# Kernel optimization log

Measured on AMD Instinct MI355X. Metric: run time of the kernel, lower is better.

The kernel has to match this reference:

```python
import jax, jax.numpy as jnp
import numpy as np

WT, WH, WW = 2, 8, 8
N_WIN = WT * WH * WW  # 128 tokens per window
DIM, HEADS = 192, 6
HEAD_DIM = DIM // HEADS
SCALE = HEAD_DIM ** -0.5


def _relative_position_index():
    ct, ch, cw = np.arange(WT), np.arange(WH), np.arange(WW)
    coords = np.stack(np.meshgrid(ct, ch, cw, indexing='ij'))  # (3,WT,WH,WW)
    cf = coords.reshape(3, -1)
    rel = cf[:, :, None] - cf[:, None, :]  # (3,N,N)
    rel = rel.transpose(1, 2, 0).copy()
    rel[:, :, 0] += WT - 1
    rel[:, :, 1] += WH - 1
    rel[:, :, 2] += WW - 1
    rel[:, :, 0] *= (2 * WH - 1) * (2 * WW - 1)
    rel[:, :, 1] *= 2 * WW - 1
    return rel.sum(-1)  # (N,N) int

_REL_IDX = jnp.asarray(_relative_position_index())


def _layernorm(x, g, b, eps=1e-5):
    mu = x.mean(-1, keepdims=True)
    var = ((x - mu) ** 2).mean(-1, keepdims=True)
    return (x - mu) * jax.lax.rsqrt(var + eps) * g + b


def setup_inputs() -> dict:
    key = jax.random.key(0)
    ks = jax.random.split(key, 16)
    B, T, H, W, C = 2, 8, 128, 128, DIM
    hid = 4 * C
    n_bias = (2 * WT - 1) * (2 * WH - 1) * (2 * WW - 1)
    s = lambda fan: 1.0 / np.sqrt(fan)
    return {
        'x': jax.random.normal(ks[0], (B, T, H, W, C), jnp.float32),
        'norm1_g': jnp.ones((C,), jnp.float32),
        'norm1_b': jnp.zeros((C,), jnp.float32),
        'qkv_w': jax.random.normal(ks[1], (3 * C, C), jnp.float32) * s(C),
        'qkv_b': jnp.zeros((3 * C,), jnp.float32),
        'bias_table': jax.random.normal(ks[2], (n_bias, HEADS), jnp.float32) * 0.02,
        'proj_w': jax.random.normal(ks[3], (C, C), jnp.float32) * s(C),
        'proj_b': jnp.zeros((C,), jnp.float32),
        'norm2_g': jnp.ones((C,), jnp.float32),
        'norm2_b': jnp.zeros((C,), jnp.float32),
        'fc1_w': jax.random.normal(ks[4], (hid, C), jnp.float32) * s(C),
        'fc1_b': jnp.zeros((hid,), jnp.float32),
        'fc2_w': jax.random.normal(ks[5], (C, hid), jnp.float32) * s(hid),
        'fc2_b': jnp.zeros((C,), jnp.float32),
    }


def reference(x, norm1_g, norm1_b, qkv_w, qkv_b, bias_table, proj_w, proj_b,
              norm2_g, norm2_b, fc1_w, fc1_b, fc2_w, fc2_b):
    B, T, H, W, C = x.shape
    shortcut = x
    xn = _layernorm(x, norm1_g, norm1_b)

    # window partition: (B,T,H,W,C) -> (B_, N, C)
    xw = xn.reshape(B, T // WT, WT, H // WH, WH, W // WW, WW, C)
    xw = xw.transpose(0, 1, 3, 5, 2, 4, 6, 7).reshape(-1, N_WIN, C)

    # qkv projection (torch Linear: y = x @ W.T + b)
    qkv = xw @ qkv_w.T + qkv_b  # (B_, N, 3C)
    B_ = qkv.shape[0]
    qkv = qkv.reshape(B_, N_WIN, 3, HEADS, HEAD_DIM)
    q, k, v = qkv[:, :, 0], qkv[:, :, 1], qkv[:, :, 2]  # (B_, N, h, d)

    attn = jnp.einsum('bnhd,bmhd->bhnm', q * SCALE, k)
    bias = bias_table[_REL_IDX.reshape(-1)].reshape(N_WIN, N_WIN, HEADS)
    attn = attn + bias.transpose(2, 0, 1)[None]  # (B_, h, N, N)
    attn = jax.nn.softmax(attn, axis=-1)

    out = jnp.einsum('bhnm,bmhd->bnhd', attn, v).reshape(B_, N_WIN, C)
    out = out @ proj_w.T + proj_b

    # window reverse
    out = out.reshape(B, T // WT, H // WH, W // WW, WT, WH, WW, C)
    out = out.transpose(0, 1, 4, 2, 5, 3, 6, 7).reshape(B, T, H, W, C)

    x = shortcut + out
    # MLP with residual (GELU exact, matching nn.GELU default)
    h1 = _layernorm(x, norm2_g, norm2_b) @ fc1_w.T + fc1_b
    h1 = jax.nn.gelu(h1, approximate=False)
    x = x + (h1 @ fc2_w.T + fc2_b)
    return x
```

## Files before the change

kernel.cpp:

```cpp
#include <hip/hip_runtime.h>
#include <hip/hip_bf16.h>
#include <math.h>

typedef __hip_bfloat16 bf16;
typedef __attribute__((ext_vector_type(8))) __bf16 bf16x8;
typedef __attribute__((ext_vector_type(4))) float floatx4;

#define CDIM 192
#define N_WINDOWS 2048
#define ATT_SCALE 0.17677669529663687f

__device__ inline float toF(float v) { return v; }
__device__ inline float toF(bf16 v) { return __bfloat162float(v); }

__device__ inline long nat_index(int wi, int n, int col) {
    int wb = wi & 15, hb = (wi >> 4) & 15, tb = (wi >> 8) & 3, bb = wi >> 10;
    int t  = tb * 2 + (n >> 6);
    int hh = hb * 8 + ((n >> 3) & 7);
    int w  = wb * 8 + (n & 7);
    return ((((long)(bb * 8 + t)) * 128 + hh) * 128 + w) * CDIM + col;
}

template<bool WINDOWED, typename T>
__launch_bounds__(256)
__global__ void ln_kernel(const T* __restrict__ x, const float* __restrict__ g,
                          const float* __restrict__ bta, bf16* __restrict__ out,
                          int wi_base) {
    int row = blockIdx.x * 4 + (threadIdx.x >> 6);
    int lane = threadIdx.x & 63;
    long src;
    if (WINDOWED) {
        src = nat_index(wi_base + (row >> 7), row & 127, 0);
    } else {
        src = (long)row * CDIM;
    }
    float v0 = toF(x[src + lane]);
    float v1 = toF(x[src + lane + 64]);
    float v2 = toF(x[src + lane + 128]);
    float s = v0 + v1 + v2;
    float sq = v0 * v0 + v1 * v1 + v2 * v2;
    #pragma unroll
    for (int o = 32; o > 0; o >>= 1) { s += __shfl_xor(s, o); sq += __shfl_xor(sq, o); }
    float mean = s * (1.0f / 192.0f);
    float var  = sq * (1.0f / 192.0f) - mean * mean;
    float rstd = rsqrtf(fmaxf(var, 0.0f) + 1e-5f);
    long dst = (long)row * CDIM;
    out[dst + lane]       = __float2bfloat16((v0 - mean) * rstd * g[lane]       + bta[lane]);
    out[dst + lane + 64]  = __float2bfloat16((v1 - mean) * rstd * g[lane + 64]  + bta[lane + 64]);
    out[dst + lane + 128] = __float2bfloat16((v2 - mean) * rstd * g[lane + 128] + bta[lane + 128]);
}

template<typename Epi>
__launch_bounds__(256)
__global__ void gemm_bt(const bf16* __restrict__ A, const float* __restrict__ Wt,
                        int K, Epi epi) {
    __shared__ __align__(16) bf16 sA[128 * 32];
    __shared__ __align__(16) bf16 sW[64 * 32];
    const int tid = threadIdx.x;
    const int lane = tid & 63;
    const int wv = tid >> 6;
    const int m0 = blockIdx.x * 128;
    const int n0 = blockIdx.y * 64;

    floatx4 acc[2][4] = {};

    for (int k0 = 0; k0 < K; k0 += 32) {
        #pragma unroll
        for (int i = 0; i < 2; ++i) {
            int idx = tid + i * 256;
            int row = idx >> 2, kc = (idx & 3) << 3;
            *(uint4*)(&sA[row * 32 + kc]) =
                *(const uint4*)(A + (long)(m0 + row) * K + k0 + kc);
        }
        {
            int row = tid >> 2, kc = (tid & 3) << 3;
            const float* wp = Wt + (long)(n0 + row) * K + k0 + kc;
            float4 w0 = *(const float4*)wp;
            float4 w1 = *(const float4*)(wp + 4);
            bf16x8 wvv;
            wvv[0] = (__bf16)w0.x; wvv[1] = (__bf16)w0.y; wvv[2] = (__bf16)w0.z; wvv[3] = (__bf16)w0.w;
            wvv[4] = (__bf16)w1.x; wvv[5] = (__bf16)w1.y; wvv[6] = (__bf16)w1.z; wvv[7] = (__bf16)w1.w;
            *(bf16x8*)(&sW[row * 32 + kc]) = wvv;
        }
        __syncthreads();
        bf16x8 aF[2], bF[4];
        #pragma unroll
        for (int rt = 0; rt < 2; ++rt)
            aF[rt] = *(const bf16x8*)(&sA[(wv * 32 + rt * 16 + (lane & 15)) * 32 + (lane >> 4) * 8]);
        #pragma unroll
        for (int ct = 0; ct < 4; ++ct)
            bF[ct] = *(const bf16x8*)(&sW[(ct * 16 + (lane & 15)) * 32 + (lane >> 4) * 8]);
        #pragma unroll
        for (int rt = 0; rt < 2; ++rt)
            #pragma unroll
            for (int ct = 0; ct < 4; ++ct)
                acc[rt][ct] = __builtin_amdgcn_mfma_f32_16x16x32_bf16(aF[rt], bF[ct], acc[rt][ct], 0, 0, 0);
        __syncthreads();
    }
    #pragma unroll
    for (int rt = 0; rt < 2; ++rt)
        #pragma unroll
        for (int ct = 0; ct < 4; ++ct)
            #pragma unroll
            for (int r = 0; r < 4; ++r) {
                int row = m0 + wv * 32 + rt * 16 + (lane >> 4) * 4 + r;
                int col = n0 + ct * 16 + (lane & 15);
                epi(row, col, acc[rt][ct][r]);
            }
}

struct EpiQKV {
    const float* bias; bf16 *q, *k, *v;
    __device__ void operator()(int row, int col, float val) const {
        val += bias[col];
        int wi = row >> 7, n = row & 127;
        int part = col / 192, rem = col - part * 192;
        int h = rem >> 5, d = rem & 31;
        long base = (long)(wi * 6 + h);
        if (part == 0)      q[(base * 128 + n) * 32 + d] = __float2bfloat16(val);
        else if (part == 1) k[(base * 128 + n) * 32 + d] = __float2bfloat16(val);
        else                v[(base * 32 + d) * 128 + n] = __float2bfloat16(val);
    }
};

struct EpiProj {
    const float* bias; const float* x; bf16* x2; int wi_base;
    __device__ void operator()(int row, int col, float val) const {
        val += bias[col];
        long nat = nat_index(wi_base + (row >> 7), row & 127, col);
        x2[(long)row * CDIM + col] = __float2bfloat16(val + x[nat]);
    }
};

struct EpiGelu {
    const float* bias; bf16* h1;
    __device__ void operator()(int row, int col, float val) const {
        val += bias[col];
        float g = 0.5f * val * (1.0f + erff(val * 0.70710678118654752f));
        h1[(long)row * 768 + col] = __float2bfloat16(g);
    }
};

struct EpiOut {
    const float* bias; const bf16* x2; float* out; int wi_base;
    __device__ void operator()(int row, int col, float val) const {
        val += bias[col];
        long nat = nat_index(wi_base + (row >> 7), row & 127, col);
        out[nat] = val + __bfloat162float(x2[(long)row * CDIM + col]);
    }
};

__device__ inline float rel_bias(const float* bt, int h, int n, int m) {
    int tn = n >> 6, hn = (n >> 3) & 7, wn = n & 7;
    int tm = m >> 6, hm = (m >> 3) & 7, wm = m & 7;
    int idx = (tn - tm + 1) * 225 + (hn - hm + 7) * 15 + (wn - wm + 7);
    return bt[idx * 6 + h];
}

__launch_bounds__(256)
__global__ void attn_kernel(const bf16* __restrict__ q, const bf16* __restrict__ k,
                            const bf16* __restrict__ vT, const float* __restrict__ bt,
                            bf16* __restrict__ out) {
    __shared__ __align__(16) bf16 sQ[128 * 32];
    __shared__ __align__(16) bf16 sK[128 * 32];
    __shared__ __align__(16) bf16 sVT[32 * 128];
    __shared__ __align__(16) bf16 sP[128 * 128];
    const int blk = blockIdx.x;
    const int h = blk % 6;
    const int wi = blk / 6;
    const int tid = threadIdx.x, lane = tid & 63, wv = tid >> 6;
    const bf16* qg = q + (long)blk * 4096;
    const bf16* kg = k + (long)blk * 4096;
    const bf16* vg = vT + (long)blk * 4096;
    #pragma unroll
    for (int i = 0; i < 2; ++i) {
        int idx = (tid + i * 256) * 8;
        *(uint4*)(&sQ[idx])  = *(const uint4*)(qg + idx);
        *(uint4*)(&sK[idx])  = *(const uint4*)(kg + idx);
        *(uint4*)(&sVT[idx]) = *(const uint4*)(vg + idx);
    }
    __syncthreads();

    const int mrow = wv * 32;
    const int colb = lane & 15, quad = lane >> 4;
    floatx4 zero = {0.f, 0.f, 0.f, 0.f};
    floatx4 s[2][8];
    bf16x8 aF[2];
    #pragma unroll
    for (int rt = 0; rt < 2; ++rt)
        aF[rt] = *(const bf16x8*)(&sQ[(mrow + rt * 16 + colb) * 32 + quad * 8]);
    #pragma unroll
    for (int ct = 0; ct < 8; ++ct) {
        bf16x8 bF = *(const bf16x8*)(&sK[(ct * 16 + colb) * 32 + quad * 8]);
        #pragma unroll
        for (int rt = 0; rt < 2; ++rt)
            s[rt][ct] = __builtin_amdgcn_mfma_f32_16x16x32_bf16(aF[rt], bF, zero, 0, 0, 0);
    }
    #pragma unroll
    for (int rt = 0; rt < 2; ++rt) {
        #pragma unroll
        for (int r = 0; r < 4; ++r) {
            int n = mrow + rt * 16 + quad * 4 + r;
            float vals[8];
            float mx = -1e30f;
            #pragma unroll
            for (int ct = 0; ct < 8; ++ct) {
                float v = s[rt][ct][r] * ATT_SCALE + rel_bias(bt, h, n, ct * 16 + colb);
                vals[ct] = v; mx = fmaxf(mx, v);
            }
            #pragma unroll
            for (int o = 1; o < 16; o <<= 1) mx = fmaxf(mx, __shfl_xor(mx, o));
            float sum = 0.f;
            #pragma unroll
            for (int ct = 0; ct < 8; ++ct) { vals[ct] = __expf(vals[ct] - mx); sum += vals[ct]; }
            #pragma unroll
            for (int o = 1; o < 16; o <<= 1) sum += __shfl_xor(sum, o);
            float inv = 1.0f / sum;
            #pragma unroll
            for (int ct = 0; ct < 8; ++ct)
                sP[n * 128 + ct * 16 + colb] = __float2bfloat16(vals[ct] * inv);
        }
    }
    __syncthreads();
    floatx4 o[2][2] = {};
    #pragma unroll
    for (int kk = 0; kk < 4; ++kk) {
        bf16x8 aP[2];
        #pragma unroll
        for (int rt = 0; rt < 2; ++rt)
            aP[rt] = *(const bf16x8*)(&sP[(mrow + rt * 16 + colb) * 128 + kk * 32 + quad * 8]);
        #pragma unroll
        for (int ct = 0; ct < 2; ++ct) {
            bf16x8 bV = *(const bf16x8*)(&sVT[(ct * 16 + colb) * 128 + kk * 32 + quad * 8]);
            #pragma unroll
            for (int rt = 0; rt < 2; ++rt)
                o[rt][ct] = __builtin_amdgcn_mfma_f32_16x16x32_bf16(aP[rt], bV, o[rt][ct], 0, 0, 0);
        }
    }
    #pragma unroll
    for (int rt = 0; rt < 2; ++rt)
        #pragma unroll
        for (int ct = 0; ct < 2; ++ct)
            #pragma unroll
            for (int r = 0; r < 4; ++r) {
                int n = mrow + rt * 16 + quad * 4 + r;
                out[((long)(wi * 128 + n)) * CDIM + h * 32 + ct * 16 + colb] =
                    __float2bfloat16(o[rt][ct][r]);
            }
}

extern "C" void kernel_launch(void* const* d_in, const int* in_sizes, int n_in,
                              void* d_out, int out_size, void* d_ws, size_t ws_size,
                              hipStream_t stream) {
    const float* x      = (const float*)d_in[0];
    const float* n1g    = (const float*)d_in[1];
    const float* n1b    = (const float*)d_in[2];
    const float* qkv_w  = (const float*)d_in[3];
    const float* qkv_b  = (const float*)d_in[4];
    const float* btab   = (const float*)d_in[5];
    const float* proj_w = (const float*)d_in[6];
    const float* proj_b = (const float*)d_in[7];
    const float* n2g    = (const float*)d_in[8];
    const float* n2b    = (const float*)d_in[9];
    const float* fc1_w  = (const float*)d_in[10];
    const float* fc1_b  = (const float*)d_in[11];
    const float* fc2_w  = (const float*)d_in[12];
    const float* fc2_b  = (const float*)d_in[13];
    float* outp = (float*)d_out;

    const size_t per_win = 6UL * 128 * 192 * 2;
    int S = N_WINDOWS;
    while (S > 64 && (size_t)S * per_win > ws_size) S >>= 1;

    char* ws = (char*)d_ws;
    const size_t SLOT = (size_t)S * 128 * CDIM * 2;
    bf16* bufA = (bf16*)(ws);
    bf16* qb   = (bf16*)(ws + SLOT);
    bf16* kb   = (bf16*)(ws + 2 * SLOT);
    bf16* vb   = (bf16*)(ws + 3 * SLOT);
    bf16* x2   = qb;
    bf16* h1   = kb;

    for (int s0 = 0; s0 < N_WINDOWS; s0 += S) {
        ln_kernel<true, float><<<S * 32, 256, 0, stream>>>(x, n1g, n1b, bufA, s0);
        gemm_bt<EpiQKV><<<dim3(S, 9), 256, 0, stream>>>(bufA, qkv_w, 192, EpiQKV{qkv_b, qb, kb, vb});
        attn_kernel<<<S * 6, 256, 0, stream>>>(qb, kb, vb, btab, bufA);
        gemm_bt<EpiProj><<<dim3(S, 3), 256, 0, stream>>>(bufA, proj_w, 192, EpiProj{proj_b, x, x2, s0});
        ln_kernel<false, bf16><<<S * 32, 256, 0, stream>>>(x2, n2g, n2b, bufA, 0);
        gemm_bt<EpiGelu><<<dim3(S, 12), 256, 0, stream>>>(bufA, fc1_w, 192, EpiGelu{fc1_b, h1});
        gemm_bt<EpiOut><<<dim3(S, 3), 256, 0, stream>>>(h1, fc2_w, 768, EpiOut{fc2_b, x2, outp, s0});
    }
}
```

Measured before the change: 1.782 ms.

## Fuse LN2+MLP into one kernel, pre-convert weights to bf16, pad LDS

Adds a one-time kernel that converts all weights to bf16 so the GEMMs load bf16 directly instead of converting fp32 on every tile. Replaces the LN2, fc1+GELU and fc2 kernels with a fused MLP kernel that keeps the hidden activations in shared memory, removing the h1 round trip through global memory. Pads LDS row strides in the GEMM and attention kernels to reduce bank conflicts. Also swaps erff for an Abramowitz-Stegun polynomial erf approximation, which adds small numerical error.

```diff
diff --git a/kernel.cpp b/kernel.cpp
--- a/kernel.cpp
+++ b/kernel.cpp
@@ -21,22 +21,43 @@
     return ((((long)(bb * 8 + t)) * 128 + hh) * 128 + w) * CDIM + col;
 }
 
-template<bool WINDOWED, typename T>
+__device__ inline float erf_as(float x) {
+    float ax = fabsf(x);
+    float t = 1.0f / (1.0f + 0.3275911f * ax);
+    float p = t * (0.254829592f + t * (-0.284496736f + t * (1.421413741f +
+              t * (-1.453152027f + t * 1.061405429f))));
+    float e = 1.0f - p * __expf(-ax * ax);
+    return copysignf(e, x);
+}
+
 __launch_bounds__(256)
-__global__ void ln_kernel(const T* __restrict__ x, const float* __restrict__ g,
+__global__ void convert_weights(const float* __restrict__ qkv_w, const float* __restrict__ proj_w,
+                                const float* __restrict__ fc1_w, const float* __restrict__ fc2_w,
+                                bf16* __restrict__ dst) {
+    long e = ((long)blockIdx.x * 256 + threadIdx.x) * 8;
+    const float* src; long off;
+    if (e < 110592)       { src = qkv_w;  off = e; }
+    else if (e < 147456)  { src = proj_w; off = e - 110592; }
+    else if (e < 294912)  { src = fc1_w;  off = e - 147456; }
+    else                  { src = fc2_w;  off = e - 294912; }
+    float4 a = *(const float4*)(src + off);
+    float4 b = *(const float4*)(src + off + 4);
+    bf16x8 o;
+    o[0] = (__bf16)a.x; o[1] = (__bf16)a.y; o[2] = (__bf16)a.z; o[3] = (__bf16)a.w;
+    o[4] = (__bf16)b.x; o[5] = (__bf16)b.y; o[6] = (__bf16)b.z; o[7] = (__bf16)b.w;
+    *(bf16x8*)(dst + e) = o;
+}
+
+__launch_bounds__(256)
+__global__ void ln_kernel(const float* __restrict__ x, const float* __restrict__ g,
                           const float* __restrict__ bta, bf16* __restrict__ out,
                           int wi_base) {
     int row = blockIdx.x * 4 + (threadIdx.x >> 6);
     int lane = threadIdx.x & 63;
-    long src;
-    if (WINDOWED) {
-        src = nat_index(wi_base + (row >> 7), row & 127, 0);
-    } else {
-        src = (long)row * CDIM;
-    }
-    float v0 = toF(x[src + lane]);
-    float v1 = toF(x[src + lane + 64]);
-    float v2 = toF(x[src + lane + 128]);
+    long src = nat_index(wi_base + (row >> 7), row & 127, 0);
+    float v0 = x[src + lane];
+    float v1 = x[src + lane + 64];
+    float v2 = x[src + lane + 128];
     float s = v0 + v1 + v2;
     float sq = v0 * v0 + v1 * v1 + v2 * v2;
     #pragma unroll
@@ -52,13 +73,14 @@
 
 template<typename Epi>
 __launch_bounds__(256)
-__global__ void gemm_bt(const bf16* __restrict__ A, const float* __restrict__ Wt,
+__global__ void gemm_bt(const bf16* __restrict__ A, const bf16* __restrict__ Wt,
                         int K, Epi epi) {
-    __shared__ __align__(16) bf16 sA[128 * 32];
-    __shared__ __align__(16) bf16 sW[64 * 32];
+    __shared__ __align__(16) bf16 sA[128 * 40];
+    __shared__ __align__(16) bf16 sW[64 * 40];
     const int tid = threadIdx.x;
     const int lane = tid & 63;
     const int wv = tid >> 6;
+    const int colb = lane & 15, quad = lane >> 4;
     const int m0 = blockIdx.x * 128;
     const int n0 = blockIdx.y * 64;
 
@@ -69,27 +91,22 @@
         for (int i = 0; i < 2; ++i) {
             int idx = tid + i * 256;
             int row = idx >> 2, kc = (idx & 3) << 3;
-            *(uint4*)(&sA[row * 32 + kc]) =
+            *(uint4*)(&sA[row * 40 + kc]) =
                 *(const uint4*)(A + (long)(m0 + row) * K + k0 + kc);
         }
         {
             int row = tid >> 2, kc = (tid & 3) << 3;
-            const float* wp = Wt + (long)(n0 + row) * K + k0 + kc;
-            float4 w0 = *(const float4*)wp;
-            float4 w1 = *(const float4*)(wp + 4);
-            bf16x8 wvv;
-            wvv[0] = (__bf16)w0.x; wvv[1] = (__bf16)w0.y; wvv[2] = (__bf16)w0.z; wvv[3] = (__bf16)w0.w;
-            wvv[4] = (__bf16)w1.x; wvv[5] = (__bf16)w1.y; wvv[6] = (__bf16)w1.z; wvv[7] = (__bf16)w1.w;
-            *(bf16x8*)(&sW[row * 32 + kc]) = wvv;
+            *(uint4*)(&sW[row * 40 + kc]) =
+                *(const uint4*)(Wt + (long)(n0 + row) * K + k0 + kc);
         }
         __syncthreads();
         bf16x8 aF[2], bF[4];
         #pragma unroll
         for (int rt = 0; rt < 2; ++rt)
-            aF[rt] = *(const bf16x8*)(&sA[(wv * 32 + rt * 16 + (lane & 15)) * 32 + (lane >> 4) * 8]);
+            aF[rt] = *(const bf16x8*)(&sA[(wv * 32 + rt * 16 + colb) * 40 + quad * 8]);
         #pragma unroll
         for (int ct = 0; ct < 4; ++ct)
-            bF[ct] = *(const bf16x8*)(&sW[(ct * 16 + (lane & 15)) * 32 + (lane >> 4) * 8]);
+            bF[ct] = *(const bf16x8*)(&sW[(ct * 16 + colb) * 40 + quad * 8]);
         #pragma unroll
         for (int rt = 0; rt < 2; ++rt)
             #pragma unroll
@@ -103,8 +120,8 @@
         for (int ct = 0; ct < 4; ++ct)
             #pragma unroll
             for (int r = 0; r < 4; ++r) {
-                int row = m0 + wv * 32 + rt * 16 + (lane >> 4) * 4 + r;
-                int col = n0 + ct * 16 + (lane & 15);
+                int row = m0 + wv * 32 + rt * 16 + quad * 4 + r;
+                int col = n0 + ct * 16 + colb;
                 epi(row, col, acc[rt][ct][r]);
             }
 }
@@ -132,24 +149,6 @@
     }
 };
 
-struct EpiGelu {
-    const float* bias; bf16* h1;
-    __device__ void operator()(int row, int col, float val) const {
-        val += bias[col];
-        float g = 0.5f * val * (1.0f + erff(val * 0.70710678118654752f));
-        h1[(long)row * 768 + col] = __float2bfloat16(g);
-    }
-};
-
-struct EpiOut {
-    const float* bias; const bf16* x2; float* out; int wi_base;
-    __device__ void operator()(int row, int col, float val) const {
-        val += bias[col];
-        long nat = nat_index(wi_base + (row >> 7), row & 127, col);
-        out[nat] = val + __bfloat162float(x2[(long)row * CDIM + col]);
-    }
-};
-
 __device__ inline float rel_bias(const float* bt, int h, int n, int m) {
     int tn = n >> 6, hn = (n >> 3) & 7, wn = n & 7;
     int tm = m >> 6, hm = (m >> 3) & 7, wm = m & 7;
@@ -161,10 +160,10 @@
 __global__ void attn_kernel(const bf16* __restrict__ q, const bf16* __restrict__ k,
                             const bf16* __restrict__ vT, const float* __restrict__ bt,
                             bf16* __restrict__ out) {
-    __shared__ __align__(16) bf16 sQ[128 * 32];
-    __shared__ __align__(16) bf16 sK[128 * 32];
-    __shared__ __align__(16) bf16 sVT[32 * 128];
-    __shared__ __align__(16) bf16 sP[128 * 128];
+    __shared__ __align__(16) bf16 sQ[128 * 40];
+    __shared__ __align__(16) bf16 sK[128 * 40];
+    __shared__ __align__(16) bf16 sVT[32 * 136];
+    __shared__ __align__(16) bf16 sP[128 * 136];
     const int blk = blockIdx.x;
     const int h = blk % 6;
     const int wi = blk / 6;
@@ -174,10 +173,12 @@
     const bf16* vg = vT + (long)blk * 4096;
     #pragma unroll
     for (int i = 0; i < 2; ++i) {
-        int idx = (tid + i * 256) * 8;
-        *(uint4*)(&sQ[idx])  = *(const uint4*)(qg + idx);
-        *(uint4*)(&sK[idx])  = *(const uint4*)(kg + idx);
-        *(uint4*)(&sVT[idx]) = *(const uint4*)(vg + idx);
+        int v = tid + i * 256;
+        int r4 = v >> 2, kc = (v & 3) << 3;
+        *(uint4*)(&sQ[r4 * 40 + kc])  = *(const uint4*)(qg + v * 8);
+        *(uint4*)(&sK[r4 * 40 + kc])  = *(const uint4*)(kg + v * 8);
+        int rv = v >> 4, cv = (v & 15) << 3;
+        *(uint4*)(&sVT[rv * 136 + cv]) = *(const uint4*)(vg + v * 8);
     }
     __syncthreads();
 
@@ -188,10 +189,10 @@
     bf16x8 aF[2];
     #pragma unroll
     for (int rt = 0; rt < 2; ++rt)
-        aF[rt] = *(const bf16x8*)(&sQ[(mrow + rt * 16 + colb) * 32 + quad * 8]);
+        aF[rt] = *(const bf16x8*)(&sQ[(mrow + rt * 16 + colb) * 40 + quad * 8]);
     #pragma unroll
     for (int ct = 0; ct < 8; ++ct) {
-        bf16x8 bF = *(const bf16x8*)(&sK[(ct * 16 + colb) * 32 + quad * 8]);
+        bf16x8 bF = *(const bf16x8*)(&sK[(ct * 16 + colb) * 40 + quad * 8]);
         #pragma unroll
         for (int rt = 0; rt < 2; ++rt)
             s[rt][ct] = __builtin_amdgcn_mfma_f32_16x16x32_bf16(aF[rt], bF, zero, 0, 0, 0);
@@ -218,7 +219,7 @@
             float inv = 1.0f / sum;
             #pragma unroll
             for (int ct = 0; ct < 8; ++ct)
-                sP[n * 128 + ct * 16 + colb] = __float2bfloat16(vals[ct] * inv);
+                sP[n * 136 + ct * 16 + colb] = __float2bfloat16(vals[ct] * inv);
         }
     }
     __syncthreads();
@@ -228,10 +229,10 @@
         bf16x8 aP[2];
         #pragma unroll
         for (int rt = 0; rt < 2; ++rt)
-            aP[rt] = *(const bf16x8*)(&sP[(mrow + rt * 16 + colb) * 128 + kk * 32 + quad * 8]);
+            aP[rt] = *(const bf16x8*)(&sP[(mrow + rt * 16 + colb) * 136 + kk * 32 + quad * 8]);
         #pragma unroll
         for (int ct = 0; ct < 2; ++ct) {
-            bf16x8 bV = *(const bf16x8*)(&sVT[(ct * 16 + colb) * 128 + kk * 32 + quad * 8]);
+            bf16x8 bV = *(const bf16x8*)(&sVT[(ct * 16 + colb) * 136 + kk * 32 + quad * 8]);
             #pragma unroll
             for (int rt = 0; rt < 2; ++rt)
                 o[rt][ct] = __builtin_amdgcn_mfma_f32_16x16x32_bf16(aP[rt], bV, o[rt][ct], 0, 0, 0);
@@ -247,6 +248,110 @@
                 out[((long)(wi * 128 + n)) * CDIM + h * 32 + ct * 16 + colb] =
                     __float2bfloat16(o[rt][ct][r]);
             }
+}
+
+__launch_bounds__(256)
+__global__ void mlp_kernel(const bf16* __restrict__ x2, const float* __restrict__ g,
+                           const float* __restrict__ b, const bf16* __restrict__ w1,
+                           const float* __restrict__ b1, const bf16* __restrict__ w2,
+                           const float* __restrict__ b2, float* __restrict__ out,
+                           int wi_base) {
+    __shared__ __align__(16) bf16 sX[64 * 200];
+    __shared__ __align__(16) bf16 sH[64 * 264];
+    __shared__ __align__(16) bf16 sW[256 * 40];
+    const int tid = threadIdx.x, lane = tid & 63, wv = tid >> 6;
+    const int colb = lane & 15, quad = lane >> 4;
+    const long row0 = (long)blockIdx.x * 64;
+
+    {
+        int rl = wv * 16 + colb;
+        const bf16* xp = x2 + (row0 + rl) * CDIM + quad * 48;
+        bf16x8 raw[6];
+        float s = 0.f, sq = 0.f;
+        #pragma unroll
+        for (int j = 0; j < 6; ++j) {
+            raw[j] = *(const bf16x8*)(xp + j * 8);
+            #pragma unroll
+            for (int e = 0; e < 8; ++e) { float f = (float)raw[j][e]; s += f; sq += f * f; }
+        }
+        s += __shfl_xor(s, 16); sq += __shfl_xor(sq, 16);
+        s += __shfl_xor(s, 32); sq += __shfl_xor(sq, 32);
+        float mean = s * (1.0f / 192.0f);
+        float var  = sq * (1.0f / 192.0f) - mean * mean;
+        float rstd = rsqrtf(fmaxf(var, 0.0f) + 1e-5f);
+        #pragma unroll
+        for (int j = 0; j < 6; ++j) {
+            bf16x8 o;
+            #pragma unroll
+            for (int e = 0; e < 8; ++e) {
+                int col = quad * 48 + j * 8 + e;
+                o[e] = (__bf16)(((float)raw[j][e] - mean) * rstd * g[col] + b[col]);
+            }
+            *(bf16x8*)(&sX[rl * 200 + quad * 48 + j * 8]) = o;
+        }
+    }
+
+    floatx4 oacc[12] = {};
+    for (int c = 0; c < 3; ++c) {
+        floatx4 hacc[16] = {};
+        for (int k0 = 0; k0 < 192; k0 += 32) {
+            __syncthreads();
+            {
+                const bf16* wp = w1 + ((long)(c * 256 + tid)) * 192 + k0;
+                #pragma unroll
+                for (int j = 0; j < 4; ++j)
+                    *(uint4*)(&sW[tid * 40 + j * 8]) = *(const uint4*)(wp + j * 8);
+            }
+            __syncthreads();
+            bf16x8 aF = *(const bf16x8*)(&sX[(wv * 16 + colb) * 200 + k0 + quad * 8]);
+            #pragma unroll
+            for (int nt = 0; nt < 16; ++nt) {
+                bf16x8 bF = *(const bf16x8*)(&sW[(nt * 16 + colb) * 40 + quad * 8]);
+                hacc[nt] = __builtin_amdgcn_mfma_f32_16x16x32_bf16(aF, bF, hacc[nt], 0, 0, 0);
+            }
+        }
+        #pragma unroll
+        for (int nt = 0; nt < 16; ++nt) {
+            float bv = b1[c * 256 + nt * 16 + colb];
+            #pragma unroll
+            for (int r = 0; r < 4; ++r) {
+                float val = hacc[nt][r] + bv;
+                float gl = 0.5f * val * (1.0f + erf_as(val * 0.70710678118654752f));
+                sH[(wv * 16 + quad * 4 + r) * 264 + nt * 16 + colb] = __float2bfloat16(gl);
+            }
+        }
+        for (int kk = 0; kk < 256; kk += 32) {
+            __syncthreads();
+            {
+                #pragma unroll
+                for (int i = 0; i < 3; ++i) {
+                    int v = tid + i * 256;
+                    int n = v >> 2, j = (v & 3) << 3;
+                    *(uint4*)(&sW[n * 40 + j]) =
+                        *(const uint4*)(w2 + (long)n * 768 + c * 256 + kk + j);
+                }
+            }
+            __syncthreads();
+            bf16x8 aF = *(const bf16x8*)(&sH[(wv * 16 + colb) * 264 + kk + quad * 8]);
+            #pragma unroll
+            for (int ot = 0; ot < 12; ++ot) {
+                bf16x8 bF = *(const bf16x8*)(&sW[(ot * 16 + colb) * 40 + quad * 8]);
+                oacc[ot] = __builtin_amdgcn_mfma_f32_16x16x32_bf16(aF, bF, oacc[ot], 0, 0, 0);
+            }
+        }
+    }
+    #pragma unroll
+    for (int ot = 0; ot < 12; ++ot) {
+        float bv = b2[ot * 16 + colb];
+        #pragma unroll
+        for (int r = 0; r < 4; ++r) {
+            long rl = row0 + wv * 16 + quad * 4 + r;
+            int col = ot * 16 + colb;
+            int wi = wi_base + (int)(rl >> 7), n = (int)rl & 127;
+            float val = oacc[ot][r] + bv + (float)x2[rl * CDIM + col];
+            out[nat_index(wi, n, col)] = val;
+        }
+    }
 }
 
 extern "C" void kernel_launch(void* const* d_in, const int* in_sizes, int n_in,
@@ -268,26 +373,33 @@
     const float* fc2_b  = (const float*)d_in[13];
     float* outp = (float*)d_out;
 
-    const size_t per_win = 6UL * 128 * 192 * 2;
+    char* ws = (char*)d_ws;
+    bf16* wts   = (bf16*)ws;
+    bf16* wqkv  = wts;
+    bf16* wproj = wts + 110592;
+    bf16* w1    = wts + 147456;
+    bf16* w2    = wts + 294912;
+    const size_t WBYTES = 442368UL * 2;
+
+    const size_t per_win = 4UL * 128 * CDIM * 2;
     int S = N_WINDOWS;
-    while (S > 64 && (size_t)S * per_win > ws_size) S >>= 1;
-
-    char* ws = (char*)d_ws;
+    while (S > 64 && (size_t)S * per_win + WBYTES > ws_size) S >>= 1;
+
+    char* sl = ws + WBYTES;
     const size_t SLOT = (size_t)S * 128 * CDIM * 2;
-    bf16* bufA = (bf16*)(ws);
-    bf16* qb   = (bf16*)(ws + SLOT);
-    bf16* kb   = (bf16*)(ws + 2 * SLOT);
-    bf16* vb   = (bf16*)(ws + 3 * SLOT);
+    bf16* bufA = (bf16*)(sl);
+    bf16* qb   = (bf16*)(sl + SLOT);
+    bf16* kb   = (bf16*)(sl + 2 * SLOT);
+    bf16* vb   = (bf16*)(sl + 3 * SLOT);
     bf16* x2   = qb;
-    bf16* h1   = kb;
+
+    convert_weights<<<216, 256, 0, stream>>>(qkv_w, proj_w, fc1_w, fc2_w, wts);
 
     for (int s0 = 0; s0 < N_WINDOWS; s0 += S) {
-        ln_kernel<true, float><<<S * 32, 256, 0, stream>>>(x, n1g, n1b, bufA, s0);
-        gemm_bt<EpiQKV><<<dim3(S, 9), 256, 0, stream>>>(bufA, qkv_w, 192, EpiQKV{qkv_b, qb, kb, vb});
+        ln_kernel<<<S * 32, 256, 0, stream>>>(x, n1g, n1b, bufA, s0);
+        gemm_bt<EpiQKV><<<dim3(S, 9), 256, 0, stream>>>(bufA, wqkv, 192, EpiQKV{qkv_b, qb, kb, vb});
         attn_kernel<<<S * 6, 256, 0, stream>>>(qb, kb, vb, btab, bufA);
-        gemm_bt<EpiProj><<<dim3(S, 3), 256, 0, stream>>>(bufA, proj_w, 192, EpiProj{proj_b, x, x2, s0});
-        ln_kernel<false, bf16><<<S * 32, 256, 0, stream>>>(x2, n2g, n2b, bufA, 0);
-        gemm_bt<EpiGelu><<<dim3(S, 12), 256, 0, stream>>>(bufA, fc1_w, 192, EpiGelu{fc1_b, h1});
-        gemm_bt<EpiOut><<<dim3(S, 3), 256, 0, stream>>>(h1, fc2_w, 768, EpiOut{fc2_b, x2, outp, s0});
-    }
-}
+        gemm_bt<EpiProj><<<dim3(S, 3), 256, 0, stream>>>(bufA, wproj, 192, EpiProj{proj_b, x, x2, s0});
+        mlp_kernel<<<S * 2, 256, 0, stream>>>(x2, n2g, n2b, w1, fc1_b, w2, fc2_b, outp, s0);
+    }
+}
```

Result: slower. 2.074 ms (+16.4%).
